# Kernel tuning notes

Hardware: AMD Instinct MI355X
Metric: run time of the kernel (lower is better)

## Reference

```python
import jax, jax.numpy as jnp
import numpy as np

TAU = 0.1          # contrastive_temperature
EPS = 0.05         # property_epsilon
L_LOCAL_G, L_GLOBAL, L_SC_G, L_LOCAL_SC, G_PROP = 1.0, 0.8, 1.0, 0.8, 0.5
B = 4096
D = 256
NUM_PROPS = 4
N_ATOMS = 131072
N_MOTIFS = 32768


def setup_inputs() -> dict:
    key = jax.random.key(0)
    ks = jax.random.split(key, 10)
    return {
        "emb_g_mole": jax.random.normal(ks[0], (B, D), jnp.float32),
        "emb_g_frag": jax.random.normal(ks[1], (N_ATOMS, D), jnp.float32),
        "emb_sc_mole": jax.random.normal(ks[2], (B, D), jnp.float32),
        "emb_sc_shape": jax.random.normal(ks[3], (N_MOTIFS, D), jnp.float32),
        "emb_motif": jax.random.normal(ks[4], (N_MOTIFS, D), jnp.float32),
        "emb_shape": jax.random.normal(ks[5], (N_MOTIFS, D), jnp.float32),
        # scaled so duplicate rows are the only pairs within EPS (realistic sparse mask)
        "prop_pred": jax.random.normal(ks[6], (B, NUM_PROPS), jnp.float32) * 0.05,
        "prop_target": jax.random.normal(ks[7], (B, NUM_PROPS), jnp.float32) * 0.05,
        "batch_g": jax.random.randint(ks[8], (N_ATOMS,), 0, B, jnp.int32),
        "batch_sc": jax.random.randint(ks[9], (N_MOTIFS,), 0, B, jnp.int32),
    }


def _contrastive(emb, props):
    # SupervisedContrastiveLoss: normalized cosine logits, mask from sqrt(cdist) < eps
    n = emb.shape[0]
    e = emb / jnp.maximum(jnp.linalg.norm(emb, axis=1, keepdims=True), 1e-12)
    logits = jnp.matmul(e, e.T) / TAU                       # [n, n]
    log_probs = jax.nn.log_softmax(logits, axis=1)
    sq = jnp.sum(props * props, axis=1)
    d2 = jnp.maximum(sq[:, None] + sq[None, :] - 2.0 * jnp.matmul(props, props.T), 0.0)
    dd = jnp.sqrt(jnp.sqrt(d2)) + 1e-8                      # cdist(...).sqrt() + 1e-8
    mask = (dd < EPS) & (~jnp.eye(n, dtype=bool))           # fill_diagonal_(0)
    cnt = jnp.sum(mask, axis=1)
    row_loss = -jnp.sum(jnp.where(mask, log_probs, 0.0), axis=1) / jnp.maximum(cnt, 1)
    valid = cnt > 0
    nvalid = jnp.sum(valid)
    loss = jnp.sum(jnp.where(valid, row_loss, 0.0)) / jnp.maximum(nvalid, 1)
    return jnp.where(nvalid > 0, loss, 0.0)


def _frag_alignment(emb_g_frag, emb_motif, batch_g, batch_sc):
    ones_g = jnp.ones((emb_g_frag.shape[0],), emb_g_frag.dtype)
    ones_s = jnp.ones((emb_motif.shape[0],), emb_motif.dtype)
    cnt_g = jax.ops.segment_sum(ones_g, batch_g, num_segments=B)
    cnt_s = jax.ops.segment_sum(ones_s, batch_sc, num_segments=B)
    mean_g = jax.ops.segment_sum(emb_g_frag, batch_g, num_segments=B) / jnp.maximum(cnt_g, 1.0)[:, None]
    mean_s = jax.ops.segment_sum(emb_motif, batch_sc, num_segments=B) / jnp.maximum(cnt_s, 1.0)[:, None]
    norms = jnp.linalg.norm(mean_g - mean_s, axis=1)
    valid = (cnt_g > 0) & (cnt_s > 0)
    batch_size = batch_g.max().astype(emb_g_frag.dtype) + 1.0
    return jnp.sum(jnp.where(valid, norms, 0.0)) / batch_size


def reference(emb_g_mole, emb_g_frag, emb_sc_mole, emb_sc_shape, emb_motif,
              emb_shape, prop_pred, prop_target, batch_g, batch_sc):
    l_local_g = _frag_alignment(emb_g_frag, emb_motif, batch_g, batch_sc)
    combined_emb = jnp.concatenate([emb_g_mole, emb_sc_mole], axis=0)    # [2B, d]
    combined_props = jnp.concatenate([prop_pred, prop_pred], axis=0)      # [2B, p]
    l_contr = _contrastive(combined_emb, combined_props)
    l_global = l_contr          # same inputs in both calls -> identical value
    l_local_sc = l_contr
    l_sc_g = jnp.mean(jnp.linalg.norm(emb_sc_shape - emb_shape, axis=1))  # AlignmentLoss mean
    l_prop = jnp.mean((prop_pred - prop_target) ** 2)                     # MSELoss
    l_hes = (L_LOCAL_G * l_local_g + L_GLOBAL * l_global + L_SC_G * l_sc_g
             + L_LOCAL_SC * l_local_sc + G_PROP * l_prop)
    # stacked: [l_hes, l_local_g, l_global, l_sc_g, l_local_sc, l_prop]
    return jnp.stack([l_hes, l_local_g, l_global, l_sc_g, l_local_sc, l_prop])
```

## Files before the change

kernel.cpp:

```cpp
#include <hip/hip_runtime.h>
#include <hip/hip_bf16.h>
#include <stdint.h>

typedef unsigned short u16;
typedef float f32x4 __attribute__((ext_vector_type(4)));
typedef short s16x8 __attribute__((ext_vector_type(8)));
typedef u16   u16x8 __attribute__((ext_vector_type(8)));
typedef u16   u16x4 __attribute__((ext_vector_type(4)));
typedef uint32_t u32x4 __attribute__((ext_vector_type(4)));

#define B_      4096
#define D_      256
#define NA_     131072
#define NM_     32768
#define N2_     8192
#define THR4    6.2499950e-6f
#define K2E     14.426950408889634f
#define CAPG    96
#define CAPS    40

#define NS_   1024
#define NG_   2080
#define NT_   256
#define NTOT_ 3360
#define NR_   2336

#define OFF_CNT_G   0u
#define OFF_CNT_S   16384u
#define OFF_NB      32768u
#define OFF_SCAL    49152u
#define OFF_S       65536u
#define ZERO_BYTES  98304u
#define OFF_T       98304u
#define OFF_C       131072u
#define OFF_PLIST   163840u
#define OFF_LIST_G  688128u
#define OFF_LIST_S  2260992u
#define OFF_E       2916352u
#define WS_NEED     7110656u

__device__ inline float wave_sum(float v) {
#pragma unroll
  for (int m = 1; m < 64; m <<= 1) v += __shfl_xor(v, m, 64);
  return v;
}
__device__ inline int wave_sum_i(int v) {
#pragma unroll
  for (int m = 1; m < 64; m <<= 1) v += __shfl_xor(v, m, 64);
  return v;
}
__device__ inline u16 f2bf(float f) {
  uint32_t u = __float_as_uint(f);
  uint32_t r = (u + 0x7FFFu + ((u >> 16) & 1u)) >> 16;
  return (u16)r;
}
__device__ inline float bf2f(u16 v) { return __uint_as_float(((uint32_t)v) << 16); }

__device__ inline f32x4 ldnt4(const float* p) {
  return __builtin_nontemporal_load((const f32x4*)p);
}

__device__ inline void gload16(const u16* __restrict__ g, u16* l) {
  __builtin_amdgcn_global_load_lds(
      (const __attribute__((address_space(1))) uint32_t*)g,
      (__attribute__((address_space(3))) uint32_t*)l, 16, 0, 0);
}

__global__ void k_zero(u32x4* __restrict__ p) {
  u32x4 z = {0u, 0u, 0u, 0u};
  p[blockIdx.x * 256 + threadIdx.x] = z;
}

__global__ __launch_bounds__(256) void k_fuseA(
    const int* __restrict__ bg, const int* __restrict__ bs,
    int* __restrict__ cntg, int* __restrict__ cnts, int* __restrict__ bmax,
    int* __restrict__ listg, int* __restrict__ lists,
    const float* __restrict__ gm, const float* __restrict__ scm,
    const float* __restrict__ scs, const float* __restrict__ shp,
    const float* __restrict__ pp,
    u16* __restrict__ E, int* __restrict__ nb, int* __restrict__ plist,
    float* __restrict__ scal) {
  int t = threadIdx.x, w = t >> 6, lane = t & 63;
  int blk = blockIdx.x;

  if (blk < 512) {
    int i = blk * 256 + t;
    int b = -1;
    if (i < NA_) {
      b = bg[i];
      int pos = atomicAdd(&cntg[b], 1);
      if (pos < CAPG) listg[b * CAPG + pos] = i;
    }
    if (i < NM_) {
      int b2 = bs[i];
      int pos = atomicAdd(&cnts[b2], 1);
      if (pos < CAPS) lists[b2 * CAPS + pos] = i;
    }
    int m = b;
#pragma unroll
    for (int k = 1; k < 64; k <<= 1) m = max(m, __shfl_xor(m, k, 64));
    if ((t & 63) == 0 && m >= 0) atomicMax(bmax, m);
  } else if (blk < 4608) {
    int a = blk - 512;
    f32x4 pa = *(const f32x4*)(pp + (size_t)a * 4);
    for (int b = t; b < B_; b += 256) {
      f32x4 pb = *(const f32x4*)(pp + (size_t)b * 4);
      float dx = pa.x - pb.x, dy = pa.y - pb.y, dz = pa.z - pb.z, dw = pa.w - pb.w;
      float d2 = dx * dx + dy * dy + dz * dz + dw * dw;
      if (d2 < THR4) {
        int pos = atomicAdd(&nb[a], 1);
        if (pos < 32) plist[a * 32 + pos] = b;
      }
    }
  } else if (blk < 6656) {
    int r = (blk - 4608) * 4 + w;
    const float* src = (r < B_) ? gm + (size_t)r * D_ : scm + (size_t)(r - B_) * D_;
    f32x4 v = ldnt4(src + lane * 4);
    float ss = v.x * v.x + v.y * v.y + v.z * v.z + v.w * v.w;
    ss = wave_sum(ss);
    float inv = 1.f / fmaxf(sqrtf(ss), 1e-12f);
    u16x4 o;
    o.x = f2bf(v.x * inv); o.y = f2bf(v.y * inv);
    o.z = f2bf(v.z * inv); o.w = f2bf(v.w * inv);
    *(u16x4*)(E + (size_t)r * D_ + lane * 4) = o;
  } else {
    int wg = (blk - 6656) * 4 + w;
    float acc = 0.f;
    for (int r = wg; r < NM_; r += 8192) {
      f32x4 va = ldnt4(scs + (size_t)r * D_ + lane * 4);
      f32x4 vb = ldnt4(shp + (size_t)r * D_ + lane * 4);
      float dx = va.x - vb.x, dy = va.y - vb.y, dz = va.z - vb.z, dw = va.w - vb.w;
      float ss = wave_sum(dx * dx + dy * dy + dz * dz + dw * dw);
      if (lane == 0) acc += sqrtf(ss);
    }
    __shared__ float sr4[4];
    if (lane == 0) sr4[w] = acc;
    __syncthreads();
    if (t == 0) atomicAdd(&scal[1], sr4[0] + sr4[1] + sr4[2] + sr4[3]);
  }
}

__device__ inline void wave_row_sum(const float* __restrict__ src,
                                    const int* __restrict__ list,
                                    int off, int cnt, int lane, f32x4* accs) {
  f32x4 a0 = {0.f,0.f,0.f,0.f}, a1 = a0, a2 = a0, a3 = a0;
  f32x4 a4 = a0, a5 = a0, a6 = a0, a7 = a0;
  for (int base = 0; base < cnt; base += 64) {
    int n = min(cnt - base, 64);
    int idx = (lane < n) ? list[off + base + lane] : 0;
    int k = 0;
    for (; k + 7 < n; k += 8) {
      int i0 = __shfl(idx, k,     64), i1 = __shfl(idx, k + 1, 64);
      int i2 = __shfl(idx, k + 2, 64), i3 = __shfl(idx, k + 3, 64);
      int i4 = __shfl(idx, k + 4, 64), i5 = __shfl(idx, k + 5, 64);
      int i6 = __shfl(idx, k + 6, 64), i7 = __shfl(idx, k + 7, 64);
      a0 += ldnt4(src + (size_t)i0 * D_ + lane * 4);
      a1 += ldnt4(src + (size_t)i1 * D_ + lane * 4);
      a2 += ldnt4(src + (size_t)i2 * D_ + lane * 4);
      a3 += ldnt4(src + (size_t)i3 * D_ + lane * 4);
      a4 += ldnt4(src + (size_t)i4 * D_ + lane * 4);
      a5 += ldnt4(src + (size_t)i5 * D_ + lane * 4);
      a6 += ldnt4(src + (size_t)i6 * D_ + lane * 4);
      a7 += ldnt4(src + (size_t)i7 * D_ + lane * 4);
    }
    for (; k < n; k++) {
      int i0 = __shfl(idx, k, 64);
      a0 += ldnt4(src + (size_t)i0 * D_ + lane * 4);
    }
  }
  *accs = ((a0 + a1) + (a2 + a3)) + ((a4 + a5) + (a6 + a7));
}

__global__ __launch_bounds__(256) void k_fuseB(
    const u16* __restrict__ E,
    const float* __restrict__ fg, const float* __restrict__ fm,
    const int* __restrict__ cntg, const int* __restrict__ cnts,
    const int* __restrict__ listg, const int* __restrict__ lists,
    const int* __restrict__ nb, const int* __restrict__ plist,
    float* __restrict__ S, float* __restrict__ T, int* __restrict__ C,
    float* __restrict__ scal) {
  __shared__ __align__(16) u16 As[128 * 64];
  __shared__ __align__(16) u16 Bs[128 * 64];
  int blk = blockIdx.x;
  int tid = threadIdx.x, lane = tid & 63, wid = tid >> 6;

  int64_t p = (int64_t)blk * NS_;
  int srem = (int)(p % NTOT_);
  if (srem < NS_) {
    int sid = (int)(p / NTOT_);
    int b = sid * 4 + wid;
    int cg = cntg[b], cs = cnts[b];
    f32x4 sg, ss;
    wave_row_sum(fg, listg, b * CAPG, min(cg, CAPG), lane, &sg);
    wave_row_sum(fm, lists, b * CAPS, min(cs, CAPS), lane, &ss);
    float ig = 1.f / fmaxf((float)cg, 1.f);
    float is = 1.f / fmaxf((float)cs, 1.f);
    float dx = sg.x * ig - ss.x * is, dy = sg.y * ig - ss.y * is;
    float dz = sg.z * ig - ss.z * is, dw = sg.w * ig - ss.w * is;
    float v = wave_sum(dx * dx + dy * dy + dz * dz + dw * dw);
    __shared__ float r2[4];
    if (lane == 0) r2[wid] = (cg > 0 && cs > 0) ? sqrtf(v) : 0.f;
    __syncthreads();
    if (tid == 0) {
      float s = r2[0] + r2[1] + r2[2] + r2[3];
      if (s != 0.f) atomicAdd(&scal[0], s);
    }
    return;
  }

  int r = blk - (int)((p + NTOT_ - 1) / NTOT_);
  int64_t q = (int64_t)r * NG_;
  int grem = (int)(q % NR_);

  if (grem >= NG_) {
    int tix = r - (int)((q + NR_ - 1) / NR_);
#pragma unroll
    for (int k8 = 0; k8 < 8; k8++) {
      int i = tix * 32 + wid * 8 + k8;
      int a = i & (B_ - 1);
      int n = min(nb[a], 32);
      u16x4 vi = *(const u16x4*)(E + (size_t)i * D_ + lane * 4);
      float ex = bf2f(vi.x), ey = bf2f(vi.y), ez = bf2f(vi.z), ew = bf2f(vi.w);
      float acc = -(ex * ex + ey * ey + ez * ez + ew * ew);
      for (int k = 0; k < n; k++) {
        int b = plist[a * 32 + k];
        u16x4 v1 = *(const u16x4*)(E + (size_t)b * D_ + lane * 4);
        u16x4 v2 = *(const u16x4*)(E + (size_t)(b + B_) * D_ + lane * 4);
        acc += ex * bf2f(v1.x) + ey * bf2f(v1.y) + ez * bf2f(v1.z) + ew * bf2f(v1.w);
        acc += ex * bf2f(v2.x) + ey * bf2f(v2.y) + ez * bf2f(v2.z) + ew * bf2f(v2.w);
      }
      acc = wave_sum(acc);
      if (lane == 0) { T[i] = 10.0f * acc; C[i] = 2 * n - 1; }
    }
    return;
  }

  int t = (int)(q / NR_);
  int bi = (int)((129.0f - sqrtf(129.0f * 129.0f - 8.0f * (float)t)) * 0.5f);
  while ((bi + 1) * (129 - (bi + 1)) / 2 <= t) bi++;
  while (bi * (129 - bi) / 2 > t) bi--;
  int bj = bi + (t - bi * (129 - bi) / 2);

  int row0 = bi * 128, col0 = bj * 128;
  int wr = wid >> 1, wc = wid & 1;

  int rsub = lane >> 3;
  int csw  = (((lane & 7) ^ rsub) << 4) >> 1;

  f32x4 acc[4][4];
#pragma unroll
  for (int mi = 0; mi < 4; mi++)
#pragma unroll
    for (int ni = 0; ni < 4; ni++) {
      f32x4 z = {0.f, 0.f, 0.f, 0.f};
      acc[mi][ni] = z;
    }

  for (int kc = 0; kc < 4; ++kc) {
    __syncthreads();
#pragma unroll
    for (int it = 0; it < 4; it++) {
      int s = wid * 4 + it;
      int rr = s * 8 + rsub;
      gload16(E + (size_t)(row0 + rr) * D_ + kc * 64 + csw, As + s * 512);
      gload16(E + (size_t)(col0 + rr) * D_ + kc * 64 + csw, Bs + s * 512);
    }
    __syncthreads();
#pragma unroll
    for (int kk = 0; kk < 2; ++kk) {
      s16x8 af[4], bfr[4];
#pragma unroll
      for (int mi = 0; mi < 4; mi++) {
        int rA = wr * 64 + mi * 16 + (lane & 15);
        int cbf = kk * 64 + (lane >> 4) * 16;
        int addr = rA * 128 + (cbf ^ ((rA & 7) << 4));
        af[mi] = *(const s16x8*)((const char*)As + addr);
      }
#pragma unroll
      for (int ni = 0; ni < 4; ni++) {
        int rB = wc * 64 + ni * 16 + (lane & 15);
        int cbf = kk * 64 + (lane >> 4) * 16;
        int addr = rB * 128 + (cbf ^ ((rB & 7) << 4));
        bfr[ni] = *(const s16x8*)((const char*)Bs + addr);
      }
#pragma unroll
      for (int mi = 0; mi < 4; mi++)
#pragma unroll
        for (int ni = 0; ni < 4; ni++)
          acc[mi][ni] = __builtin_amdgcn_mfma_f32_16x16x32_bf16(af[mi], bfr[ni], acc[mi][ni], 0, 0, 0);
    }
  }

  int g = lane >> 4, cl = lane & 15;
  float colsum[4] = {0.f, 0.f, 0.f, 0.f};
#pragma unroll
  for (int mi = 0; mi < 4; mi++) {
#pragma unroll
    for (int reg = 0; reg < 4; ++reg) {
      int gi = row0 + wr * 64 + mi * 16 + g * 4 + reg;
      float vs = 0.f;
#pragma unroll
      for (int ni = 0; ni < 4; ni++) {
        float e = exp2f(acc[mi][ni][reg] * K2E - K2E);
        vs += e;
        colsum[ni] += e;
      }
#pragma unroll
      for (int m = 1; m < 16; m <<= 1) vs += __shfl_xor(vs, m, 64);
      if (cl == 0) atomicAdd(&S[gi], vs);
    }
  }
  if (bi != bj) {
#pragma unroll
    for (int ni = 0; ni < 4; ni++) {
      float cs = colsum[ni];
      cs += __shfl_xor(cs, 16, 64);
      cs += __shfl_xor(cs, 32, 64);
      if (g == 0) atomicAdd(&S[col0 + wc * 64 + ni * 16 + cl], cs);
    }
  }
}

__global__ void k_final(const float* __restrict__ S, const float* __restrict__ T,
                        const int* __restrict__ C, const float* __restrict__ scal,
                        const float* __restrict__ pp, const float* __restrict__ pt,
                        float* __restrict__ out) {
  float sp = 0.f;
  for (int i = threadIdx.x; i < B_ * 4; i += 256) {
    float d = pp[i] - pt[i];
    sp += d * d;
  }
  float rls = 0.f; int nv = 0;
  for (int i = threadIdx.x; i < N2_; i += 256) {
    int ci = C[i];
    if (ci > 0) { rls += (10.0f + logf(S[i])) - T[i] / (float)ci; nv++; }
  }
  rls = wave_sum(rls);
  sp  = wave_sum(sp);
  nv  = wave_sum_i(nv);
  __shared__ float r1[4], r3[4]; __shared__ int r2[4];
  int lane = threadIdx.x & 63, w = threadIdx.x >> 6;
  if (lane == 0) { r1[w] = rls; r2[w] = nv; r3[w] = sp; }
  __syncthreads();
  if (threadIdx.x == 0) {
    float rtot = r1[0] + r1[1] + r1[2] + r1[3];
    int nvt = r2[0] + r2[1] + r2[2] + r2[3];
    float sptot = r3[0] + r3[1] + r3[2] + r3[3];
    float l_contr = nvt > 0 ? rtot / (float)nvt : 0.f;
    int bmax = ((const int*)scal)[3];
    float bs = (float)bmax + 1.0f;
    float l_local_g = scal[0] / bs;
    float l_sc = scal[1] / (float)NM_;
    float l_prop = sptot / (float)(B_ * 4);
    float l_hes = 1.0f * l_local_g + 0.8f * l_contr + 1.0f * l_sc + 0.8f * l_contr + 0.5f * l_prop;
    out[0] = l_hes; out[1] = l_local_g; out[2] = l_contr;
    out[3] = l_sc;  out[4] = l_contr;   out[5] = l_prop;
  }
}

extern "C" void kernel_launch(void* const* d_in, const int* in_sizes, int n_in,
                              void* d_out, int out_size, void* d_ws, size_t ws_size,
                              hipStream_t stream) {
  if (ws_size < WS_NEED) return;
  const float* gm  = (const float*)d_in[0];
  const float* fg  = (const float*)d_in[1];
  const float* scm = (const float*)d_in[2];
  const float* scs = (const float*)d_in[3];
  const float* mot = (const float*)d_in[4];
  const float* shp = (const float*)d_in[5];
  const float* pp  = (const float*)d_in[6];
  const float* pt  = (const float*)d_in[7];
  const int* bg = (const int*)d_in[8];
  const int* bs = (const int*)d_in[9];
  float* out = (float*)d_out;
  char* ws = (char*)d_ws;

  int* cntg  = (int*)(ws + OFF_CNT_G);
  int* cnts  = (int*)(ws + OFF_CNT_S);
  int* nb    = (int*)(ws + OFF_NB);
  float* scal = (float*)(ws + OFF_SCAL);
  float* S   = (float*)(ws + OFF_S);
  float* T   = (float*)(ws + OFF_T);
  int* C     = (int*)(ws + OFF_C);
  int* plist = (int*)(ws + OFF_PLIST);
  int* listg = (int*)(ws + OFF_LIST_G);
  int* lists = (int*)(ws + OFF_LIST_S);
  u16* E     = (u16*)(ws + OFF_E);

  k_zero<<<24, 256, 0, stream>>>((u32x4*)ws);
  k_fuseA<<<8704, 256, 0, stream>>>(bg, bs, cntg, cnts, (int*)scal + 3,
                                    listg, lists, gm, scm, scs, shp, pp,
                                    E, nb, plist, scal);
  k_fuseB<<<NTOT_, 256, 0, stream>>>(E, fg, mot, cntg, cnts, listg, lists,
                                     nb, plist, S, T, C, scal);
  k_final<<<1, 256, 0, stream>>>(S, T, C, scal, pp, pt, out);
}
```

Measured before the change: 202.8 us.

## Split Gram tiles into 128x64 halves and load MFMA operands directly from global

The symmetric Gram-matrix part of the fused kernel now splits each 128x128 upper-triangular tile into two 128x64 sub-tiles, doubling the number of GEMM blocks. It also drops the LDS staging path (global_load_lds plus swizzled shared reads and barriers), so each wave reads its bf16 fragments straight from global/L2 memory. The intent is more parallelism and no LDS or synchronisation overhead. The cost is less operand reuse, more L2 traffic from uncoalesced 16-byte row loads, and a second set of column-sum atomics per tile.

Result: slower. 266.2 us (+31.3%).

```diff
diff --git a/kernel.cpp b/kernel.cpp
--- a/kernel.cpp
+++ b/kernel.cpp
@@ -20,10 +20,10 @@
 #define CAPS    40
 
 #define NS_   1024
-#define NG_   2080
+#define NG_   4160
 #define NT_   256
-#define NTOT_ 3360
-#define NR_   2336
+#define NTOT_ 5440
+#define NR_   4416
 
 #define OFF_CNT_G   0u
 #define OFF_CNT_S   16384u
@@ -57,13 +57,7 @@
 __device__ inline float bf2f(u16 v) { return __uint_as_float(((uint32_t)v) << 16); }
 
 __device__ inline f32x4 ldnt4(const float* p) {
-  return __builtin_nontemporal_load((const f32x4*)p);
-}
-
-__device__ inline void gload16(const u16* __restrict__ g, u16* l) {
-  __builtin_amdgcn_global_load_lds(
-      (const __attribute__((address_space(1))) uint32_t*)g,
-      (__attribute__((address_space(3))) uint32_t*)l, 16, 0, 0);
+  return __builtin_nontemporal_load((const f32x4*)(p));
 }
 
 __global__ void k_zero(u32x4* __restrict__ p) {
@@ -179,8 +173,6 @@
     const int* __restrict__ nb, const int* __restrict__ plist,
     float* __restrict__ S, float* __restrict__ T, int* __restrict__ C,
     float* __restrict__ scal) {
-  __shared__ __align__(16) u16 As[128 * 64];
-  __shared__ __align__(16) u16 Bs[128 * 64];
   int blk = blockIdx.x;
   int tid = threadIdx.x, lane = tid & 63, wid = tid >> 6;
 
@@ -235,64 +227,46 @@
     return;
   }
 
-  int t = (int)(q / NR_);
+  int gid = (int)(q / NR_);
+  int t = gid >> 1, sub = gid & 1;
   int bi = (int)((129.0f - sqrtf(129.0f * 129.0f - 8.0f * (float)t)) * 0.5f);
   while ((bi + 1) * (129 - (bi + 1)) / 2 <= t) bi++;
   while (bi * (129 - bi) / 2 > t) bi--;
   int bj = bi + (t - bi * (129 - bi) / 2);
 
-  int row0 = bi * 128, col0 = bj * 128;
+  int row0 = bi * 128, col0 = bj * 128 + sub * 64;
   int wr = wid >> 1, wc = wid & 1;
-
-  int rsub = lane >> 3;
-  int csw  = (((lane & 7) ^ rsub) << 4) >> 1;
-
-  f32x4 acc[4][4];
+  int rl = lane & 15, g = lane >> 4;
+
+  const u16* Abase = E + (size_t)(row0 + wr * 64 + rl) * D_ + g * 8;
+  const u16* Bbase = E + (size_t)(col0 + wc * 32 + rl) * D_ + g * 8;
+
+  f32x4 acc[4][2];
 #pragma unroll
   for (int mi = 0; mi < 4; mi++)
 #pragma unroll
-    for (int ni = 0; ni < 4; ni++) {
+    for (int ni = 0; ni < 2; ni++) {
       f32x4 z = {0.f, 0.f, 0.f, 0.f};
       acc[mi][ni] = z;
     }
 
-  for (int kc = 0; kc < 4; ++kc) {
-    __syncthreads();
-#pragma unroll
-    for (int it = 0; it < 4; it++) {
-      int s = wid * 4 + it;
-      int rr = s * 8 + rsub;
-      gload16(E + (size_t)(row0 + rr) * D_ + kc * 64 + csw, As + s * 512);
-      gload16(E + (size_t)(col0 + rr) * D_ + kc * 64 + csw, Bs + s * 512);
-    }
-    __syncthreads();
-#pragma unroll
-    for (int kk = 0; kk < 2; ++kk) {
-      s16x8 af[4], bfr[4];
-#pragma unroll
-      for (int mi = 0; mi < 4; mi++) {
-        int rA = wr * 64 + mi * 16 + (lane & 15);
-        int cbf = kk * 64 + (lane >> 4) * 16;
-        int addr = rA * 128 + (cbf ^ ((rA & 7) << 4));
-        af[mi] = *(const s16x8*)((const char*)As + addr);
-      }
-#pragma unroll
-      for (int ni = 0; ni < 4; ni++) {
-        int rB = wc * 64 + ni * 16 + (lane & 15);
-        int cbf = kk * 64 + (lane >> 4) * 16;
-        int addr = rB * 128 + (cbf ^ ((rB & 7) << 4));
-        bfr[ni] = *(const s16x8*)((const char*)Bs + addr);
-      }
-#pragma unroll
-      for (int mi = 0; mi < 4; mi++)
-#pragma unroll
-        for (int ni = 0; ni < 4; ni++)
-          acc[mi][ni] = __builtin_amdgcn_mfma_f32_16x16x32_bf16(af[mi], bfr[ni], acc[mi][ni], 0, 0, 0);
-    }
-  }
-
-  int g = lane >> 4, cl = lane & 15;
-  float colsum[4] = {0.f, 0.f, 0.f, 0.f};
+  for (int ko = 0; ko < 8; ++ko) {
+    int k0 = ko * 32;
+    s16x8 af[4], bfr[2];
+#pragma unroll
+    for (int mi = 0; mi < 4; mi++)
+      af[mi] = *(const s16x8*)(Abase + (size_t)mi * 16 * D_ + k0);
+#pragma unroll
+    for (int ni = 0; ni < 2; ni++)
+      bfr[ni] = *(const s16x8*)(Bbase + (size_t)ni * 16 * D_ + k0);
+#pragma unroll
+    for (int mi = 0; mi < 4; mi++)
+#pragma unroll
+      for (int ni = 0; ni < 2; ni++)
+        acc[mi][ni] = __builtin_amdgcn_mfma_f32_16x16x32_bf16(af[mi], bfr[ni], acc[mi][ni], 0, 0, 0);
+  }
+
+  float colsum[2] = {0.f, 0.f};
 #pragma unroll
   for (int mi = 0; mi < 4; mi++) {
 #pragma unroll
@@ -300,23 +274,23 @@
       int gi = row0 + wr * 64 + mi * 16 + g * 4 + reg;
       float vs = 0.f;
 #pragma unroll
-      for (int ni = 0; ni < 4; ni++) {
+      for (int ni = 0; ni < 2; ni++) {
         float e = exp2f(acc[mi][ni][reg] * K2E - K2E);
         vs += e;
         colsum[ni] += e;
       }
 #pragma unroll
       for (int m = 1; m < 16; m <<= 1) vs += __shfl_xor(vs, m, 64);
-      if (cl == 0) atomicAdd(&S[gi], vs);
+      if (rl == 0) atomicAdd(&S[gi], vs);
     }
   }
   if (bi != bj) {
 #pragma unroll
-    for (int ni = 0; ni < 4; ni++) {
+    for (int ni = 0; ni < 2; ni++) {
       float cs = colsum[ni];
       cs += __shfl_xor(cs, 16, 64);
       cs += __shfl_xor(cs, 32, 64);
-      if (g == 0) atomicAdd(&S[col0 + wc * 64 + ni * 16 + cl], cs);
+      if (g == 0) atomicAdd(&S[col0 + wc * 32 + ni * 16 + rl], cs);
     }
   }
 }
```

## Move pair-mask and shape-alignment work from fuseA into interleaved fuseB blocks

Applied to the files above, without the earlier changes.

Removes the property-pair neighbor-list stage and the emb_sc_shape/emb_shape alignment reduction from k_fuseA, leaving it with only the batch histograms and embedding normalization. The neighbor scan now runs inside k_fuseB using a wave ballot over the 4096 property rows and accumulates positive logits for both the graph and shape copies in one pass, which removes the nb/plist workspace. The alignment reduction also runs as extra fuseB blocks, interleaved with the segment-sum and GEMM tiles. This shortens the serial first kernel and overlaps the memory-bound work with the MFMA tiles, at the cost of each pair block scanning all 4096 rows.

Result: slower. 243.6 us (+20.1%).

```diff
diff --git a/kernel.cpp b/kernel.cpp
--- a/kernel.cpp
+++ b/kernel.cpp
@@ -22,22 +22,22 @@
 #define NS_   1024
 #define NG_   2080
 #define NT_   256
-#define NTOT_ 3360
-#define NR_   2336
+#define NL_   2048
+#define NTOT_ 5408
+#define NR1_  4384
+#define NR2_  2304
 
 #define OFF_CNT_G   0u
 #define OFF_CNT_S   16384u
-#define OFF_NB      32768u
-#define OFF_SCAL    49152u
-#define OFF_S       65536u
-#define ZERO_BYTES  98304u
-#define OFF_T       98304u
-#define OFF_C       131072u
-#define OFF_PLIST   163840u
-#define OFF_LIST_G  688128u
-#define OFF_LIST_S  2260992u
-#define OFF_E       2916352u
-#define WS_NEED     7110656u
+#define OFF_SCAL    32768u
+#define OFF_S       49152u
+#define ZERO_BYTES  81920u
+#define OFF_T       81920u
+#define OFF_C       114688u
+#define OFF_LIST_G  147456u
+#define OFF_LIST_S  1720320u
+#define OFF_E       2375680u
+#define WS_NEED     6569984u
 
 __device__ inline float wave_sum(float v) {
 #pragma unroll
@@ -57,7 +57,7 @@
 __device__ inline float bf2f(u16 v) { return __uint_as_float(((uint32_t)v) << 16); }
 
 __device__ inline f32x4 ldnt4(const float* p) {
-  return __builtin_nontemporal_load((const f32x4*)p);
+  return __builtin_nontemporal_load((const f32x4*)(p));
 }
 
 __device__ inline void gload16(const u16* __restrict__ g, u16* l) {
@@ -76,10 +76,7 @@
     int* __restrict__ cntg, int* __restrict__ cnts, int* __restrict__ bmax,
     int* __restrict__ listg, int* __restrict__ lists,
     const float* __restrict__ gm, const float* __restrict__ scm,
-    const float* __restrict__ scs, const float* __restrict__ shp,
-    const float* __restrict__ pp,
-    u16* __restrict__ E, int* __restrict__ nb, int* __restrict__ plist,
-    float* __restrict__ scal) {
+    u16* __restrict__ E) {
   int t = threadIdx.x, w = t >> 6, lane = t & 63;
   int blk = blockIdx.x;
 
@@ -100,20 +97,8 @@
 #pragma unroll
     for (int k = 1; k < 64; k <<= 1) m = max(m, __shfl_xor(m, k, 64));
     if ((t & 63) == 0 && m >= 0) atomicMax(bmax, m);
-  } else if (blk < 4608) {
-    int a = blk - 512;
-    f32x4 pa = *(const f32x4*)(pp + (size_t)a * 4);
-    for (int b = t; b < B_; b += 256) {
-      f32x4 pb = *(const f32x4*)(pp + (size_t)b * 4);
-      float dx = pa.x - pb.x, dy = pa.y - pb.y, dz = pa.z - pb.z, dw = pa.w - pb.w;
-      float d2 = dx * dx + dy * dy + dz * dz + dw * dw;
-      if (d2 < THR4) {
-        int pos = atomicAdd(&nb[a], 1);
-        if (pos < 32) plist[a * 32 + pos] = b;
-      }
-    }
-  } else if (blk < 6656) {
-    int r = (blk - 4608) * 4 + w;
+  } else {
+    int r = (blk - 512) * 4 + w;
     const float* src = (r < B_) ? gm + (size_t)r * D_ : scm + (size_t)(r - B_) * D_;
     f32x4 v = ldnt4(src + lane * 4);
     float ss = v.x * v.x + v.y * v.y + v.z * v.z + v.w * v.w;
@@ -123,20 +108,6 @@
     o.x = f2bf(v.x * inv); o.y = f2bf(v.y * inv);
     o.z = f2bf(v.z * inv); o.w = f2bf(v.w * inv);
     *(u16x4*)(E + (size_t)r * D_ + lane * 4) = o;
-  } else {
-    int wg = (blk - 6656) * 4 + w;
-    float acc = 0.f;
-    for (int r = wg; r < NM_; r += 8192) {
-      f32x4 va = ldnt4(scs + (size_t)r * D_ + lane * 4);
-      f32x4 vb = ldnt4(shp + (size_t)r * D_ + lane * 4);
-      float dx = va.x - vb.x, dy = va.y - vb.y, dz = va.z - vb.z, dw = va.w - vb.w;
-      float ss = wave_sum(dx * dx + dy * dy + dz * dz + dw * dw);
-      if (lane == 0) acc += sqrtf(ss);
-    }
-    __shared__ float sr4[4];
-    if (lane == 0) sr4[w] = acc;
-    __syncthreads();
-    if (t == 0) atomicAdd(&scal[1], sr4[0] + sr4[1] + sr4[2] + sr4[3]);
   }
 }
 
@@ -176,7 +147,8 @@
     const float* __restrict__ fg, const float* __restrict__ fm,
     const int* __restrict__ cntg, const int* __restrict__ cnts,
     const int* __restrict__ listg, const int* __restrict__ lists,
-    const int* __restrict__ nb, const int* __restrict__ plist,
+    const float* __restrict__ scs, const float* __restrict__ shp,
+    const float* __restrict__ pp,
     float* __restrict__ S, float* __restrict__ T, int* __restrict__ C,
     float* __restrict__ scal) {
   __shared__ __align__(16) u16 As[128 * 64];
@@ -184,10 +156,9 @@
   int blk = blockIdx.x;
   int tid = threadIdx.x, lane = tid & 63, wid = tid >> 6;
 
-  int64_t p = (int64_t)blk * NS_;
-  int srem = (int)(p % NTOT_);
-  if (srem < NS_) {
-    int sid = (int)(p / NTOT_);
+  int64_t p1 = (int64_t)blk * NS_;
+  if ((int)(p1 % NTOT_) < NS_) {
+    int sid = (int)(p1 / NTOT_);
     int b = sid * 4 + wid;
     int cg = cntg[b], cs = cnts[b];
     f32x4 sg, ss;
@@ -198,126 +169,166 @@
     float dx = sg.x * ig - ss.x * is, dy = sg.y * ig - ss.y * is;
     float dz = sg.z * ig - ss.z * is, dw = sg.w * ig - ss.w * is;
     float v = wave_sum(dx * dx + dy * dy + dz * dz + dw * dw);
-    __shared__ float r2[4];
-    if (lane == 0) r2[wid] = (cg > 0 && cs > 0) ? sqrtf(v) : 0.f;
+    __shared__ float sred[4];
+    if (lane == 0) sred[wid] = (cg > 0 && cs > 0) ? sqrtf(v) : 0.f;
     __syncthreads();
     if (tid == 0) {
-      float s = r2[0] + r2[1] + r2[2] + r2[3];
+      float s = sred[0] + sred[1] + sred[2] + sred[3];
       if (s != 0.f) atomicAdd(&scal[0], s);
     }
     return;
   }
-
-  int r = blk - (int)((p + NTOT_ - 1) / NTOT_);
-  int64_t q = (int64_t)r * NG_;
-  int grem = (int)(q % NR_);
-
-  if (grem >= NG_) {
-    int tix = r - (int)((q + NR_ - 1) / NR_);
-#pragma unroll
-    for (int k8 = 0; k8 < 8; k8++) {
-      int i = tix * 32 + wid * 8 + k8;
-      int a = i & (B_ - 1);
-      int n = min(nb[a], 32);
-      u16x4 vi = *(const u16x4*)(E + (size_t)i * D_ + lane * 4);
-      float ex = bf2f(vi.x), ey = bf2f(vi.y), ez = bf2f(vi.z), ew = bf2f(vi.w);
-      float acc = -(ex * ex + ey * ey + ez * ez + ew * ew);
-      for (int k = 0; k < n; k++) {
-        int b = plist[a * 32 + k];
-        u16x4 v1 = *(const u16x4*)(E + (size_t)b * D_ + lane * 4);
-        u16x4 v2 = *(const u16x4*)(E + (size_t)(b + B_) * D_ + lane * 4);
-        acc += ex * bf2f(v1.x) + ey * bf2f(v1.y) + ez * bf2f(v1.z) + ew * bf2f(v1.w);
-        acc += ex * bf2f(v2.x) + ey * bf2f(v2.y) + ez * bf2f(v2.z) + ew * bf2f(v2.w);
-      }
-      acc = wave_sum(acc);
-      if (lane == 0) { T[i] = 10.0f * acc; C[i] = 2 * n - 1; }
+  int r1 = blk - (int)((p1 + NTOT_ - 1) / NTOT_);
+
+  int64_t p2 = (int64_t)r1 * NG_;
+  if ((int)(p2 % NR1_) < NG_) {
+    int t = (int)(p2 / NR1_);
+    int bi = (int)((129.0f - sqrtf(129.0f * 129.0f - 8.0f * (float)t)) * 0.5f);
+    while ((bi + 1) * (129 - (bi + 1)) / 2 <= t) bi++;
+    while (bi * (129 - bi) / 2 > t) bi--;
+    int bj = bi + (t - bi * (129 - bi) / 2);
+
+    int row0 = bi * 128, col0 = bj * 128;
+    int wr = wid >> 1, wc = wid & 1;
+    int rsub = lane >> 3;
+    int csw  = (((lane & 7) ^ rsub) << 4) >> 1;
+
+    f32x4 acc[4][4];
+#pragma unroll
+    for (int mi = 0; mi < 4; mi++)
+#pragma unroll
+      for (int ni = 0; ni < 4; ni++) {
+        f32x4 z = {0.f, 0.f, 0.f, 0.f};
+        acc[mi][ni] = z;
+      }
+
+    for (int kc = 0; kc < 4; ++kc) {
+      __syncthreads();
+#pragma unroll
+      for (int it = 0; it < 4; it++) {
+        int s = wid * 4 + it;
+        int rr = s * 8 + rsub;
+        gload16(E + (size_t)(row0 + rr) * D_ + kc * 64 + csw, As + s * 512);
+        gload16(E + (size_t)(col0 + rr) * D_ + kc * 64 + csw, Bs + s * 512);
+      }
+      __syncthreads();
+#pragma unroll
+      for (int kk = 0; kk < 2; ++kk) {
+        s16x8 af[4], bfr[4];
+#pragma unroll
+        for (int mi = 0; mi < 4; mi++) {
+          int rA = wr * 64 + mi * 16 + (lane & 15);
+          int cbf = kk * 64 + (lane >> 4) * 16;
+          int addr = rA * 128 + (cbf ^ ((rA & 7) << 4));
+          af[mi] = *(const s16x8*)((const char*)As + addr);
+        }
+#pragma unroll
+        for (int ni = 0; ni < 4; ni++) {
+          int rB = wc * 64 + ni * 16 + (lane & 15);
+          int cbf = kk * 64 + (lane >> 4) * 16;
+          int addr = rB * 128 + (cbf ^ ((rB & 7) << 4));
+          bfr[ni] = *(const s16x8*)((const char*)Bs + addr);
+        }
+#pragma unroll
+        for (int mi = 0; mi < 4; mi++)
+#pragma unroll
+          for (int ni = 0; ni < 4; ni++)
+            acc[mi][ni] = __builtin_amdgcn_mfma_f32_16x16x32_bf16(af[mi], bfr[ni], acc[mi][ni], 0, 0, 0);
+      }
+    }
+
+    int g = lane >> 4, cl = lane & 15;
+    float colsum[4] = {0.f, 0.f, 0.f, 0.f};
+#pragma unroll
+    for (int mi = 0; mi < 4; mi++) {
+#pragma unroll
+      for (int reg = 0; reg < 4; ++reg) {
+        int gi = row0 + wr * 64 + mi * 16 + g * 4 + reg;
+        float vs = 0.f;
+#pragma unroll
+        for (int ni = 0; ni < 4; ni++) {
+          float e = exp2f(acc[mi][ni][reg] * K2E - K2E);
+          vs += e;
+          colsum[ni] += e;
+        }
+#pragma unroll
+        for (int m = 1; m < 16; m <<= 1) vs += __shfl_xor(vs, m, 64);
+        if (cl == 0) atomicAdd(&S[gi], vs);
+      }
+    }
+    if (bi != bj) {
+#pragma unroll
+      for (int ni = 0; ni < 4; ni++) {
+        float cs = colsum[ni];
+        cs += __shfl_xor(cs, 16, 64);
+        cs += __shfl_xor(cs, 32, 64);
+        if (g == 0) atomicAdd(&S[col0 + wc * 64 + ni * 16 + cl], cs);
+      }
     }
     return;
   }
-
-  int t = (int)(q / NR_);
-  int bi = (int)((129.0f - sqrtf(129.0f * 129.0f - 8.0f * (float)t)) * 0.5f);
-  while ((bi + 1) * (129 - (bi + 1)) / 2 <= t) bi++;
-  while (bi * (129 - bi) / 2 > t) bi--;
-  int bj = bi + (t - bi * (129 - bi) / 2);
-
-  int row0 = bi * 128, col0 = bj * 128;
-  int wr = wid >> 1, wc = wid & 1;
-
-  int rsub = lane >> 3;
-  int csw  = (((lane & 7) ^ rsub) << 4) >> 1;
-
-  f32x4 acc[4][4];
-#pragma unroll
-  for (int mi = 0; mi < 4; mi++)
-#pragma unroll
-    for (int ni = 0; ni < 4; ni++) {
-      f32x4 z = {0.f, 0.f, 0.f, 0.f};
-      acc[mi][ni] = z;
-    }
-
-  for (int kc = 0; kc < 4; ++kc) {
+  int r2 = r1 - (int)((p2 + NR1_ - 1) / NR1_);
+
+  int64_t p3 = (int64_t)r2 * NT_;
+  if ((int)(p3 % NR2_) < NT_) {
+    int tix = (int)(p3 / NR2_);
+#pragma unroll
+    for (int j = 0; j < 4; j++) {
+      int a = tix * 16 + wid * 4 + j;
+      f32x4 pa = *(const f32x4*)(pp + (size_t)a * 4);
+      u16x4 va = *(const u16x4*)(E + (size_t)a * D_ + lane * 4);
+      u16x4 vb = *(const u16x4*)(E + (size_t)(a + B_) * D_ + lane * 4);
+      float ax = bf2f(va.x), ay = bf2f(va.y), az = bf2f(va.z), aw = bf2f(va.w);
+      float bx = bf2f(vb.x), by = bf2f(vb.y), bz = bf2f(vb.z), bw = bf2f(vb.w);
+      float accA = -(ax * ax + ay * ay + az * az + aw * aw);
+      float accB = -(bx * bx + by * by + bz * bz + bw * bw);
+      int cnt = 0;
+      for (int base = 0; base < B_; base += 64) {
+        int b = base + lane;
+        f32x4 pb = *(const f32x4*)(pp + (size_t)b * 4);
+        float dx = pa.x - pb.x, dy = pa.y - pb.y, dz = pa.z - pb.z, dw = pa.w - pb.w;
+        float d2 = dx * dx + dy * dy + dz * dz + dw * dw;
+        unsigned long long m = __ballot(d2 < THR4);
+        cnt += __popcll(m);
+        while (m) {
+          int hb = __ffsll((unsigned long long)m) - 1;
+          m &= m - 1;
+          int bb = base + hb;
+          u16x4 v1 = *(const u16x4*)(E + (size_t)bb * D_ + lane * 4);
+          u16x4 v2 = *(const u16x4*)(E + (size_t)(bb + B_) * D_ + lane * 4);
+          float c1x = bf2f(v1.x), c1y = bf2f(v1.y), c1z = bf2f(v1.z), c1w = bf2f(v1.w);
+          float c2x = bf2f(v2.x), c2y = bf2f(v2.y), c2z = bf2f(v2.z), c2w = bf2f(v2.w);
+          accA += ax * c1x + ay * c1y + az * c1z + aw * c1w;
+          accA += ax * c2x + ay * c2y + az * c2z + aw * c2w;
+          accB += bx * c1x + by * c1y + bz * c1z + bw * c1w;
+          accB += bx * c2x + by * c2y + bz * c2z + bw * c2w;
+        }
+      }
+      accA = wave_sum(accA);
+      accB = wave_sum(accB);
+      if (lane == 0) {
+        T[a]      = 10.0f * accA;  C[a]      = 2 * cnt - 1;
+        T[a + B_] = 10.0f * accB;  C[a + B_] = 2 * cnt - 1;
+      }
+    }
+    return;
+  }
+  int lid = r2 - (int)((p3 + NR2_ - 1) / NR2_);
+
+  {
+    int wg = lid * 4 + wid;
+    float acc = 0.f;
+    for (int r = wg; r < NM_; r += 8192) {
+      f32x4 va = ldnt4(scs + (size_t)r * D_ + lane * 4);
+      f32x4 vb = ldnt4(shp + (size_t)r * D_ + lane * 4);
+      float dx = va.x - vb.x, dy = va.y - vb.y, dz = va.z - vb.z, dw = va.w - vb.w;
+      float ss = wave_sum(dx * dx + dy * dy + dz * dz + dw * dw);
+      if (lane == 0) acc += sqrtf(ss);
+    }
+    __shared__ float sr4[4];
+    if (lane == 0) sr4[wid] = acc;
     __syncthreads();
-#pragma unroll
-    for (int it = 0; it < 4; it++) {
-      int s = wid * 4 + it;
-      int rr = s * 8 + rsub;
-      gload16(E + (size_t)(row0 + rr) * D_ + kc * 64 + csw, As + s * 512);
-      gload16(E + (size_t)(col0 + rr) * D_ + kc * 64 + csw, Bs + s * 512);
-    }
-    __syncthreads();
-#pragma unroll
-    for (int kk = 0; kk < 2; ++kk) {
-      s16x8 af[4], bfr[4];
-#pragma unroll
-      for (int mi = 0; mi < 4; mi++) {
-        int rA = wr * 64 + mi * 16 + (lane & 15);
-        int cbf = kk * 64 + (lane >> 4) * 16;
-        int addr = rA * 128 + (cbf ^ ((rA & 7) << 4));
-        af[mi] = *(const s16x8*)((const char*)As + addr);
-      }
-#pragma unroll
-      for (int ni = 0; ni < 4; ni++) {
-        int rB = wc * 64 + ni * 16 + (lane & 15);
-        int cbf = kk * 64 + (lane >> 4) * 16;
-        int addr = rB * 128 + (cbf ^ ((rB & 7) << 4));
-        bfr[ni] = *(const s16x8*)((const char*)Bs + addr);
-      }
-#pragma unroll
-      for (int mi = 0; mi < 4; mi++)
-#pragma unroll
-        for (int ni = 0; ni < 4; ni++)
-          acc[mi][ni] = __builtin_amdgcn_mfma_f32_16x16x32_bf16(af[mi], bfr[ni], acc[mi][ni], 0, 0, 0);
-    }
-  }
-
-  int g = lane >> 4, cl = lane & 15;
-  float colsum[4] = {0.f, 0.f, 0.f, 0.f};
-#pragma unroll
-  for (int mi = 0; mi < 4; mi++) {
-#pragma unroll
-    for (int reg = 0; reg < 4; ++reg) {
-      int gi = row0 + wr * 64 + mi * 16 + g * 4 + reg;
-      float vs = 0.f;
-#pragma unroll
-      for (int ni = 0; ni < 4; ni++) {
-        float e = exp2f(acc[mi][ni][reg] * K2E - K2E);
-        vs += e;
-        colsum[ni] += e;
-      }
-#pragma unroll
-      for (int m = 1; m < 16; m <<= 1) vs += __shfl_xor(vs, m, 64);
-      if (cl == 0) atomicAdd(&S[gi], vs);
-    }
-  }
-  if (bi != bj) {
-#pragma unroll
-    for (int ni = 0; ni < 4; ni++) {
-      float cs = colsum[ni];
-      cs += __shfl_xor(cs, 16, 64);
-      cs += __shfl_xor(cs, 32, 64);
-      if (g == 0) atomicAdd(&S[col0 + wc * 64 + ni * 16 + cl], cs);
-    }
+    if (tid == 0) atomicAdd(&scal[1], sr4[0] + sr4[1] + sr4[2] + sr4[3]);
   }
 }
 
@@ -377,21 +388,18 @@
 
   int* cntg  = (int*)(ws + OFF_CNT_G);
   int* cnts  = (int*)(ws + OFF_CNT_S);
-  int* nb    = (int*)(ws + OFF_NB);
   float* scal = (float*)(ws + OFF_SCAL);
   float* S   = (float*)(ws + OFF_S);
   float* T   = (float*)(ws + OFF_T);
   int* C     = (int*)(ws + OFF_C);
-  int* plist = (int*)(ws + OFF_PLIST);
   int* listg = (int*)(ws + OFF_LIST_G);
   int* lists = (int*)(ws + OFF_LIST_S);
   u16* E     = (u16*)(ws + OFF_E);
 
-  k_zero<<<24, 256, 0, stream>>>((u32x4*)ws);
-  k_fuseA<<<8704, 256, 0, stream>>>(bg, bs, cntg, cnts, (int*)scal + 3,
-                                    listg, lists, gm, scm, scs, shp, pp,
-                                    E, nb, plist, scal);
+  k_zero<<<20, 256, 0, stream>>>((u32x4*)ws);
+  k_fuseA<<<2560, 256, 0, stream>>>(bg, bs, cntg, cnts, (int*)scal + 3,
+                                    listg, lists, gm, scm, E);
   k_fuseB<<<NTOT_, 256, 0, stream>>>(E, fg, mot, cntg, cnts, listg, lists,
-                                     nb, plist, S, T, C, scal);
+                                     scs, shp, pp, S, T, C, scal);
   k_final<<<1, 256, 0, stream>>>(S, T, C, scal, pp, pt, out);
 }
```
